# Optimization experiments

Measured on AMD Instinct MI355X. Metric: run time of the kernel, lower is better.

The kernel has to match this reference:

```python
import jax, jax.numpy as jnp
import numpy as np

N_LABELS = 89
HIDDEN = 512
WORD_EMB = 300
BATCH = 1024
IN_DIM = 2 * HIDDEN + WORD_EMB  # 1324


def _rank_weights(n):
    # rw[0] = 1; rw[i] = rw[i-1] + (1/i + 1)  (exact parenthesization of the torch code)
    rw = np.zeros(n, dtype=np.float64)
    rw[0] = 1.0
    for i in range(1, n):
        rw[i] = rw[i - 1] + (1.0 / i + 1.0)
    return jnp.asarray(rw, dtype=jnp.float32)


def setup_inputs() -> dict:
    key = jax.random.key(0)
    k1, k2, k3, k4, k5, k6 = jax.random.split(key, 6)
    ctx_rep = jax.random.normal(k1, (N_LABELS, BATCH, 2 * HIDDEN), dtype=jnp.float32)
    men_rep = jax.random.normal(k2, (BATCH, WORD_EMB), dtype=jnp.float32)
    types_emb = jax.random.normal(k3, (N_LABELS, WORD_EMB), dtype=jnp.float32)
    # trans Linear params (torch convention: weight is (out, in)); scaled like init_linear
    W_trans = jax.random.normal(k4, (WORD_EMB, IN_DIM), dtype=jnp.float32) * 0.05
    b_trans = jax.random.normal(k5, (WORD_EMB,), dtype=jnp.float32) * 0.05
    target = jax.random.randint(k6, (BATCH, N_LABELS), 0, 2, dtype=jnp.int32)
    return {"ctx_rep": ctx_rep, "men_rep": men_rep, "types_emb": types_emb,
            "W_trans": W_trans, "b_trans": b_trans, "target": target}


def _get_scores(ctx_rep, men_rep, types_emb, W_trans, b_trans):
    T, B, _ = ctx_rep.shape
    men = jnp.broadcast_to(men_rep[None], (T, B, men_rep.shape[1]))
    ctx_men = jnp.concatenate([ctx_rep, men], axis=2)            # (T, B, 1324)
    h = jax.nn.relu(jnp.einsum('tbd,ed->tbe', ctx_men, W_trans) + b_trans)  # (T, B, E)
    # dropout omitted (p=0 / eval mode for a deterministic reference)
    scores = jnp.einsum('tbe,te->tb', h, types_emb)              # (T, B)
    return scores.T                                               # (B, T)


def reference(ctx_rep, men_rep, types_emb, W_trans, b_trans, target):
    scores = _get_scores(ctx_rep, men_rep, types_emb, W_trans, b_trans)  # (B, n)
    B, n = scores.shape
    rw = _rank_weights(n)
    pos = (target == 1)
    neg = (target == 0)

    # bigger[i, j] = #{k : target[i,k]==0 and 1 - s[i,j] + s[i,k] > 0}
    viol = (1.0 + scores[:, None, :] - scores[:, :, None]) > 0.0         # (B, j, k)
    bigger = jnp.sum(viol & neg[:, None, :], axis=2)                     # (B, n)
    # r_j = bigger - 1; Python list negative indexing: rank_weights[-1] == rank_weights[n-1]
    r = (bigger - 1) % n
    w_lbl = rw[r] * pos.astype(scores.dtype)                             # weight per positive label

    # positives packed first (in label order) into slots, zero-padded -> index 0
    sorted_idx = jnp.argsort(jnp.where(pos, 0, 1), axis=1, stable=True)  # (B, n)
    pos_count = jnp.sum(pos, axis=1)
    slot = jnp.arange(n)[None, :]
    valid = slot < pos_count[:, None]
    pos_indices = jnp.where(valid, sorted_idx, 0)
    weight = jnp.where(valid, jnp.take_along_axis(w_lbl, sorted_idx, axis=1), 0.0)

    pos_values = jnp.take_along_axis(scores, pos_indices, axis=1)        # (B, n)
    neg_mask = neg.astype(scores.dtype)
    margin = jnp.maximum((1.0 + scores[:, None, :] - pos_values[:, :, None])
                         * neg_mask[:, None, :], 0.0)                    # (B, slot, k)
    loss = jnp.sum(margin * weight[:, :, None]) / B
    return loss
```

## Files before the change

kernel.cpp:

```cpp
#include <hip/hip_runtime.h>
#include <hip/hip_bf16.h>

#define NT 89
#define NB 1024
#define NE 300
#define K1 1024
#define NDIM 1324

#define BM 128
#define BN 160
#define BK 32
#define SA 40

typedef short s8 __attribute__((ext_vector_type(8)));
typedef float f4 __attribute__((ext_vector_type(4)));

static __device__ inline unsigned bf16r(float x) {
    unsigned u = __float_as_uint(x);
    u += 0x7FFFu + ((u >> 16) & 1u);
    return u >> 16;
}
static __device__ inline unsigned pack2(float x, float y) {
    return bf16r(x) | (bf16r(y) << 16);
}

__launch_bounds__(256, 2)
__global__ void scores_mfma_kernel(const float* __restrict__ ctx,
                                   const float* __restrict__ men,
                                   const float* __restrict__ W,
                                   const float* __restrict__ types,
                                   const float* __restrict__ bias,
                                   float* __restrict__ scores) {
    const int t  = blockIdx.z;
    const int b0 = blockIdx.x * BM;
    const int e0 = blockIdx.y * BN;
    const int tid = threadIdx.x;

    __shared__ unsigned short As[BM * SA];
    __shared__ unsigned short Bs[BN * SA];

    const int lane = tid & 63;
    const int wave = tid >> 6;
    const int wm = wave >> 1;
    const int wn = wave & 1;
    const int col = lane & 15;
    const int quad = lane >> 4;

    f4 acc[4][5];
    #pragma unroll
    for (int i = 0; i < 4; ++i)
        #pragma unroll
        for (int j = 0; j < 5; ++j) acc[i][j] = (f4)0.0f;

    const float* ctx_base = ctx + ((size_t)t * NB + b0) * K1;

    for (int kt = 0; kt < K1 / BK; ++kt) {
        const int k0 = kt * BK;
        __syncthreads();
        #pragma unroll
        for (int p = 0; p < 4; ++p) {
            int id = p * 256 + tid;
            int row = id >> 3, kv = id & 7;
            float4 v = *(const float4*)(ctx_base + (size_t)row * K1 + k0 + kv * 4);
            unsigned* dst = (unsigned*)&As[row * SA + kv * 4];
            dst[0] = pack2(v.x, v.y);
            dst[1] = pack2(v.z, v.w);
        }
        #pragma unroll
        for (int p = 0; p < 5; ++p) {
            int id = p * 256 + tid;
            int row = id >> 3, kv = id & 7;
            int e = e0 + row;
            float4 v = make_float4(0.f, 0.f, 0.f, 0.f);
            if (e < NE) v = *(const float4*)(W + (size_t)e * NDIM + k0 + kv * 4);
            unsigned* dst = (unsigned*)&Bs[row * SA + kv * 4];
            dst[0] = pack2(v.x, v.y);
            dst[1] = pack2(v.z, v.w);
        }
        __syncthreads();

        s8 af[4], bf[5];
        #pragma unroll
        for (int i = 0; i < 4; ++i)
            af[i] = *(const s8*)&As[(wm * 64 + i * 16 + col) * SA + quad * 8];
        #pragma unroll
        for (int j = 0; j < 5; ++j)
            bf[j] = *(const s8*)&Bs[(wn * 80 + j * 16 + col) * SA + quad * 8];
        #pragma unroll
        for (int i = 0; i < 4; ++i)
            #pragma unroll
            for (int j = 0; j < 5; ++j)
                acc[i][j] = __builtin_amdgcn_mfma_f32_16x16x32_bf16(af[i], bf[j], acc[i][j], 0, 0, 0);
    }

    for (int kt = 0; kt < 10; ++kt) {
        const int kd0 = kt * BK;
        __syncthreads();
        #pragma unroll
        for (int p = 0; p < 4; ++p) {
            int id = p * 256 + tid;
            int row = id >> 3, kv = id & 7;
            int kd = kd0 + kv * 4;
            float4 v = make_float4(0.f, 0.f, 0.f, 0.f);
            if (kd < NE) v = *(const float4*)(men + (size_t)(b0 + row) * NE + kd);
            unsigned* dst = (unsigned*)&As[row * SA + kv * 4];
            dst[0] = pack2(v.x, v.y);
            dst[1] = pack2(v.z, v.w);
        }
        #pragma unroll
        for (int p = 0; p < 5; ++p) {
            int id = p * 256 + tid;
            int row = id >> 3, kv = id & 7;
            int e = e0 + row;
            int kd = kd0 + kv * 4;
            float4 v = make_float4(0.f, 0.f, 0.f, 0.f);
            if (e < NE && kd < NE) v = *(const float4*)(W + (size_t)e * NDIM + K1 + kd);
            unsigned* dst = (unsigned*)&Bs[row * SA + kv * 4];
            dst[0] = pack2(v.x, v.y);
            dst[1] = pack2(v.z, v.w);
        }
        __syncthreads();

        s8 af[4], bf[5];
        #pragma unroll
        for (int i = 0; i < 4; ++i)
            af[i] = *(const s8*)&As[(wm * 64 + i * 16 + col) * SA + quad * 8];
        #pragma unroll
        for (int j = 0; j < 5; ++j)
            bf[j] = *(const s8*)&Bs[(wn * 80 + j * 16 + col) * SA + quad * 8];
        #pragma unroll
        for (int i = 0; i < 4; ++i)
            #pragma unroll
            for (int j = 0; j < 5; ++j)
                acc[i][j] = __builtin_amdgcn_mfma_f32_16x16x32_bf16(af[i], bf[j], acc[i][j], 0, 0, 0);
    }

    float rowsum[4][4];
    #pragma unroll
    for (int i = 0; i < 4; ++i)
        #pragma unroll
        for (int r = 0; r < 4; ++r) rowsum[i][r] = 0.0f;

    #pragma unroll
    for (int j = 0; j < 5; ++j) {
        int e = e0 + wn * 80 + j * 16 + col;
        float tv = 0.0f, bv = 0.0f;
        if (e < NE) {
            tv = types[(size_t)t * NE + e];
            bv = bias[e];
        }
        #pragma unroll
        for (int i = 0; i < 4; ++i) {
            #pragma unroll
            for (int r = 0; r < 4; ++r) {
                float h = fmaxf(acc[i][j][r] + bv, 0.0f);
                rowsum[i][r] = fmaf(h, tv, rowsum[i][r]);
            }
        }
    }
    #pragma unroll
    for (int i = 0; i < 4; ++i)
        #pragma unroll
        for (int r = 0; r < 4; ++r) {
            float v = rowsum[i][r];
            #pragma unroll
            for (int off = 1; off < 16; off <<= 1) v += __shfl_xor(v, off);
            if (col == 0) {
                int row = b0 + wm * 64 + i * 16 + quad * 4 + r;
                atomicAdd(&scores[(size_t)t * NB + row], v);
            }
        }
}

__global__ void loss_kernel(const float* __restrict__ scores,
                            const int* __restrict__ target,
                            float* __restrict__ out) {
    const int i = blockIdx.x;
    const int j = threadIdx.x;
    __shared__ float s[NT];
    __shared__ float rw[NT];
    __shared__ int   tg[NT];
    if (j < NT) {
        s[j]  = scores[(size_t)j * NB + i];
        tg[j] = target[(size_t)i * NT + j];
        float h = 0.0f;
        for (int q = 1; q <= j; ++q) h += 1.0f / (float)q;
        rw[j] = 1.0f + (float)j + h;
    }
    __syncthreads();

    float contrib = 0.0f;
    if (j < NT && tg[j] == 1) {
        const float sj = s[j];
        int bigger = 0;
        float msum = 0.0f;
        for (int k = 0; k < NT; ++k) {
            if (tg[k] == 0) {
                float v = 1.0f + s[k] - sj;
                if (v > 0.0f) { bigger++; msum += v; }
            }
        }
        int r = (bigger + NT - 1) % NT;
        contrib = rw[r] * msum;
    }
    #pragma unroll
    for (int off = 1; off < 64; off <<= 1) contrib += __shfl_xor(contrib, off);
    __shared__ float wsum[2];
    if ((threadIdx.x & 63) == 0) wsum[threadIdx.x >> 6] = contrib;
    __syncthreads();
    if (threadIdx.x == 0) atomicAdd(out, (wsum[0] + wsum[1]) * (1.0f / (float)NB));
}

extern "C" void kernel_launch(void* const* d_in, const int* in_sizes, int n_in,
                              void* d_out, int out_size, void* d_ws, size_t ws_size,
                              hipStream_t stream) {
    const float* ctx   = (const float*)d_in[0];
    const float* men   = (const float*)d_in[1];
    const float* types = (const float*)d_in[2];
    const float* W     = (const float*)d_in[3];
    const float* bias  = (const float*)d_in[4];
    const int*   tgt   = (const int*)d_in[5];
    float* out = (float*)d_out;

    float* scores = (float*)d_ws;

    (void)hipMemsetAsync(d_out, 0, sizeof(float), stream);
    (void)hipMemsetAsync(scores, 0, (size_t)NT * NB * sizeof(float), stream);
    hipLaunchKernelGGL(scores_mfma_kernel, dim3(NB / BM, 2, NT), dim3(256), 0, stream,
                       ctx, men, W, types, bias, scores);
    hipLaunchKernelGGL(loss_kernel, dim3(NB), dim3(128), 0, stream,
                       scores, tgt, out);
}
```

Baseline: 768.8 us.

## Precompute mention projection once and stream pre-packed bf16 weights without LDS

The mention part of the projection (men·W_men + bias) is identical across all 89 labels, so it is computed once by a separate kernel and used to initialise the accumulators, cutting the GEMM K dimension from 1324 to 1024. W is pre-converted to bf16 in a global buffer by another kernel. The main kernel now covers all 320 padded output columns in one 512-thread block, so each ctx row is read only once instead of twice, and operands are loaded straight from global memory into registers with no shared-memory staging or barriers. The trade-offs are reliance on cache for reuse of W across waves, uncoalesced strided per-lane ctx loads, and two extra kernel launches.

```diff
diff --git a/kernel.cpp b/kernel.cpp
--- a/kernel.cpp
+++ b/kernel.cpp
@@ -4,16 +4,15 @@
 #define NT 89
 #define NB 1024
 #define NE 300
+#define EP 320
 #define K1 1024
 #define NDIM 1324
 
-#define BM 128
-#define BN 160
-#define BK 32
-#define SA 40
-
 typedef short s8 __attribute__((ext_vector_type(8)));
 typedef float f4 __attribute__((ext_vector_type(4)));
+
+__device__ unsigned short g_Wp[EP * K1];
+__device__ float          g_M[NB * EP];
 
 static __device__ inline unsigned bf16r(float x) {
     unsigned u = __float_as_uint(x);
@@ -24,68 +23,87 @@
     return bf16r(x) | (bf16r(y) << 16);
 }
 
-__launch_bounds__(256, 2)
-__global__ void scores_mfma_kernel(const float* __restrict__ ctx,
-                                   const float* __restrict__ men,
-                                   const float* __restrict__ W,
+__global__ void pack_w_kernel(const float* __restrict__ W) {
+    int idx = blockIdx.x * 256 + threadIdx.x;
+    int e = idx >> 10, k = idx & 1023;
+    float v = (e < NE) ? W[(size_t)e * NDIM + k] : 0.0f;
+    g_Wp[idx] = (unsigned short)bf16r(v);
+}
+
+__global__ void prep_m_kernel(const float* __restrict__ men,
+                              const float* __restrict__ W,
+                              const float* __restrict__ bias) {
+    const int et = threadIdx.x & 63, bt = threadIdx.x >> 6;
+    const int e = blockIdx.y * 64 + et;
+    const int b = blockIdx.x * 4 + bt;
+    float acc = 0.0f;
+    if (e < NE) {
+        acc = bias[e];
+        const float* wr = W + (size_t)e * NDIM + K1;
+        const float* mr = men + (size_t)b * NE;
+        for (int k = 0; k < NE; k += 4) {
+            float4 wv = *(const float4*)(wr + k);
+            float4 mv = *(const float4*)(mr + k);
+            acc += wv.x * mv.x + wv.y * mv.y + wv.z * mv.z + wv.w * mv.w;
+        }
+    }
+    g_M[(size_t)b * EP + e] = acc;
+}
+
+__launch_bounds__(512, 2)
+__global__ void scores_main_kernel(const float* __restrict__ ctx,
                                    const float* __restrict__ types,
-                                   const float* __restrict__ bias,
                                    float* __restrict__ scores) {
-    const int t  = blockIdx.z;
-    const int b0 = blockIdx.x * BM;
-    const int e0 = blockIdx.y * BN;
+    const int t   = blockIdx.y;
+    const int b0  = blockIdx.x * 128;
     const int tid = threadIdx.x;
-
-    __shared__ unsigned short As[BM * SA];
-    __shared__ unsigned short Bs[BN * SA];
-
     const int lane = tid & 63;
     const int wave = tid >> 6;
-    const int wm = wave >> 1;
-    const int wn = wave & 1;
-    const int col = lane & 15;
+    const int wm = wave >> 2;
+    const int wn = wave & 3;
+    const int col  = lane & 15;
     const int quad = lane >> 4;
 
     f4 acc[4][5];
+    {
+        const float* mbase = g_M + (size_t)(b0 + wm * 64 + quad * 4) * EP + wn * 80 + col;
+        #pragma unroll
+        for (int i = 0; i < 4; ++i)
+            #pragma unroll
+            for (int j = 0; j < 5; ++j)
+                #pragma unroll
+                for (int r = 0; r < 4; ++r)
+                    acc[i][j][r] = mbase[(size_t)(i * 16 + r) * EP + j * 16];
+    }
+
+    const float* ap[4];
     #pragma unroll
     for (int i = 0; i < 4; ++i)
-        #pragma unroll
-        for (int j = 0; j < 5; ++j) acc[i][j] = (f4)0.0f;
-
-    const float* ctx_base = ctx + ((size_t)t * NB + b0) * K1;
-
-    for (int kt = 0; kt < K1 / BK; ++kt) {
-        const int k0 = kt * BK;
-        __syncthreads();
-        #pragma unroll
-        for (int p = 0; p < 4; ++p) {
-            int id = p * 256 + tid;
-            int row = id >> 3, kv = id & 7;
-            float4 v = *(const float4*)(ctx_base + (size_t)row * K1 + k0 + kv * 4);
-            unsigned* dst = (unsigned*)&As[row * SA + kv * 4];
-            dst[0] = pack2(v.x, v.y);
-            dst[1] = pack2(v.z, v.w);
-        }
-        #pragma unroll
-        for (int p = 0; p < 5; ++p) {
-            int id = p * 256 + tid;
-            int row = id >> 3, kv = id & 7;
-            int e = e0 + row;
-            float4 v = make_float4(0.f, 0.f, 0.f, 0.f);
-            if (e < NE) v = *(const float4*)(W + (size_t)e * NDIM + k0 + kv * 4);
-            unsigned* dst = (unsigned*)&Bs[row * SA + kv * 4];
-            dst[0] = pack2(v.x, v.y);
-            dst[1] = pack2(v.z, v.w);
-        }
-        __syncthreads();
-
-        s8 af[4], bf[5];
-        #pragma unroll
-        for (int i = 0; i < 4; ++i)
-            af[i] = *(const s8*)&As[(wm * 64 + i * 16 + col) * SA + quad * 8];
+        ap[i] = ctx + ((size_t)t * NB + b0 + wm * 64 + i * 16 + col) * K1 + quad * 8;
+    const unsigned short* bp[5];
+    #pragma unroll
+    for (int j = 0; j < 5; ++j)
+        bp[j] = g_Wp + (size_t)(wn * 80 + j * 16 + col) * K1 + quad * 8;
+
+    #pragma unroll 8
+    for (int kt = 0; kt < 32; ++kt) {
+        const int k = kt * 32;
+        s8 bf[5];
         #pragma unroll
         for (int j = 0; j < 5; ++j)
-            bf[j] = *(const s8*)&Bs[(wn * 80 + j * 16 + col) * SA + quad * 8];
+            bf[j] = *(const s8*)(bp[j] + k);
+        s8 af[4];
+        #pragma unroll
+        for (int i = 0; i < 4; ++i) {
+            float4 v0 = *(const float4*)(ap[i] + k);
+            float4 v1 = *(const float4*)(ap[i] + k + 4);
+            union { s8 v; unsigned u[4]; } c;
+            c.u[0] = pack2(v0.x, v0.y);
+            c.u[1] = pack2(v0.z, v0.w);
+            c.u[2] = pack2(v1.x, v1.y);
+            c.u[3] = pack2(v1.z, v1.w);
+            af[i] = c.v;
+        }
         #pragma unroll
         for (int i = 0; i < 4; ++i)
             #pragma unroll
@@ -93,70 +111,21 @@
                 acc[i][j] = __builtin_amdgcn_mfma_f32_16x16x32_bf16(af[i], bf[j], acc[i][j], 0, 0, 0);
     }
 
-    for (int kt = 0; kt < 10; ++kt) {
-        const int kd0 = kt * BK;
-        __syncthreads();
-        #pragma unroll
-        for (int p = 0; p < 4; ++p) {
-            int id = p * 256 + tid;
-            int row = id >> 3, kv = id & 7;
-            int kd = kd0 + kv * 4;
-            float4 v = make_float4(0.f, 0.f, 0.f, 0.f);
-            if (kd < NE) v = *(const float4*)(men + (size_t)(b0 + row) * NE + kd);
-            unsigned* dst = (unsigned*)&As[row * SA + kv * 4];
-            dst[0] = pack2(v.x, v.y);
-            dst[1] = pack2(v.z, v.w);
-        }
-        #pragma unroll
-        for (int p = 0; p < 5; ++p) {
-            int id = p * 256 + tid;
-            int row = id >> 3, kv = id & 7;
-            int e = e0 + row;
-            int kd = kd0 + kv * 4;
-            float4 v = make_float4(0.f, 0.f, 0.f, 0.f);
-            if (e < NE && kd < NE) v = *(const float4*)(W + (size_t)e * NDIM + K1 + kd);
-            unsigned* dst = (unsigned*)&Bs[row * SA + kv * 4];
-            dst[0] = pack2(v.x, v.y);
-            dst[1] = pack2(v.z, v.w);
-        }
-        __syncthreads();
-
-        s8 af[4], bf[5];
+    float rowsum[4][4];
+    #pragma unroll
+    for (int i = 0; i < 4; ++i)
+        #pragma unroll
+        for (int r = 0; r < 4; ++r) rowsum[i][r] = 0.0f;
+
+    #pragma unroll
+    for (int j = 0; j < 5; ++j) {
+        int e = wn * 80 + j * 16 + col;
+        float tv = (e < NE) ? types[(size_t)t * NE + e] : 0.0f;
         #pragma unroll
         for (int i = 0; i < 4; ++i)
-            af[i] = *(const s8*)&As[(wm * 64 + i * 16 + col) * SA + quad * 8];
-        #pragma unroll
-        for (int j = 0; j < 5; ++j)
-            bf[j] = *(const s8*)&Bs[(wn * 80 + j * 16 + col) * SA + quad * 8];
-        #pragma unroll
-        for (int i = 0; i < 4; ++i)
-            #pragma unroll
-            for (int j = 0; j < 5; ++j)
-                acc[i][j] = __builtin_amdgcn_mfma_f32_16x16x32_bf16(af[i], bf[j], acc[i][j], 0, 0, 0);
-    }
-
-    float rowsum[4][4];
-    #pragma unroll
-    for (int i = 0; i < 4; ++i)
-        #pragma unroll
-        for (int r = 0; r < 4; ++r) rowsum[i][r] = 0.0f;
-
-    #pragma unroll
-    for (int j = 0; j < 5; ++j) {
-        int e = e0 + wn * 80 + j * 16 + col;
-        float tv = 0.0f, bv = 0.0f;
-        if (e < NE) {
-            tv = types[(size_t)t * NE + e];
-            bv = bias[e];
-        }
-        #pragma unroll
-        for (int i = 0; i < 4; ++i) {
-            #pragma unroll
-            for (int r = 0; r < 4; ++r) {
-                float h = fmaxf(acc[i][j][r] + bv, 0.0f);
-                rowsum[i][r] = fmaf(h, tv, rowsum[i][r]);
-            }
-        }
+            #pragma unroll
+            for (int r = 0; r < 4; ++r)
+                rowsum[i][r] = fmaf(fmaxf(acc[i][j][r], 0.0f), tv, rowsum[i][r]);
     }
     #pragma unroll
     for (int i = 0; i < 4; ++i)
@@ -226,8 +195,11 @@
 
     (void)hipMemsetAsync(d_out, 0, sizeof(float), stream);
     (void)hipMemsetAsync(scores, 0, (size_t)NT * NB * sizeof(float), stream);
-    hipLaunchKernelGGL(scores_mfma_kernel, dim3(NB / BM, 2, NT), dim3(256), 0, stream,
-                       ctx, men, W, types, bias, scores);
+    hipLaunchKernelGGL(pack_w_kernel, dim3((EP * K1) / 256), dim3(256), 0, stream, W);
+    hipLaunchKernelGGL(prep_m_kernel, dim3(NB / 4, EP / 64), dim3(256), 0, stream,
+                       men, W, bias);
+    hipLaunchKernelGGL(scores_main_kernel, dim3(NB / 128, NT), dim3(512), 0, stream,
+                       ctx, types, scores);
     hipLaunchKernelGGL(loss_kernel, dim3(NB), dim3(128), 0, stream,
                        scores, tgt, out);
 }
```

Result: slower. 892.6 us (+16.1%).
